# Kernel optimization log

Hardware: AMD Instinct MI355X
Metric: run time of the kernel (lower is better)

Reference implementation:

```python
import jax, jax.numpy as jnp
import numpy as np

ROWS, COLS, BATCH, NC, DEG = 256, 512, 512, 5, 16
N = (ROWS + COLS) * BATCH            # total nodes
E = ROWS * DEG * BATCH               # total edges
EPS = 1e-07

def _idx_sets():
    blk = np.arange(BATCH)[:, None] * (ROWS + COLS)
    idx_check = (blk + np.arange(ROWS)[None, :]).ravel()          # index_one
    idx_var = (blk + ROWS + np.arange(COLS)[None, :]).ravel()      # index_two
    return jnp.asarray(idx_check, jnp.int32), jnp.asarray(idx_var, jnp.int32)

IDX_CHECK, IDX_VAR = _idx_sets()

def setup_inputs() -> dict:
    key = jax.random.key(0)
    ks = jax.random.split(key, 18)
    rng = np.random.default_rng(0)
    # per-graph block offsets; row0 = check node ids, row1 = variable ids BEFORE the +ROWS shift
    offs = np.repeat(np.arange(BATCH) * (ROWS + COLS), ROWS * DEG)
    src = offs + rng.integers(0, ROWS, size=E)
    dst = offs + rng.integers(0, COLS, size=E)
    edge_index = jnp.asarray(np.stack([src, dst]), jnp.int32)
    x = jax.random.normal(ks[0], (N, 1), jnp.float32)

    def p(k, shape, fan):
        return (jax.random.uniform(k, shape, jnp.float32) * 2.0 - 1.0) / np.sqrt(fan)

    inp = {"x": x, "edge_index": edge_index}
    for li, base in ((1, 1), (2, 9)):
        inp[f"w1_{li}"] = p(ks[base + 0], (10, 2), 2)
        inp[f"b1_{li}"] = p(ks[base + 1], (10,), 2)
        inp[f"w2_{li}"] = p(ks[base + 2], (1, 10), 10)
        inp[f"b2_{li}"] = p(ks[base + 3], (1,), 10)
        inp[f"wih_{li}"] = p(ks[base + 4], (3, 1), 1)
        inp[f"whh_{li}"] = p(ks[base + 5], (3, 1), 1)
        inp[f"bih_{li}"] = p(ks[base + 6], (3,), 1)
        inp[f"bhh_{li}"] = p(ks[base + 7], (3,), 1)
    return inp

def _ggc(h, j_idx, i_idx, agg_idx, upd_idx, w1, b1, w2, b2, wih, whh, bih, bhh):
    # message: mlp(cat[x_j, x_i])
    feat = jnp.concatenate([h[j_idx], h[i_idx]], axis=1)          # [E,2]
    hid = jax.nn.relu(feat @ w1.T + b1)                            # [E,10]
    msg = hid @ w2.T + b2                                          # [E,1]
    m = jax.ops.segment_sum(msg, agg_idx, num_segments=N)          # scatter-add -> [N,1]
    # GRUCell(input=h[idx], hx=m[idx])   (note: original passes old state as INPUT, message as HIDDEN)
    xg = h[upd_idx]
    hx = m[upd_idx]
    gi = xg @ wih.T + bih                                          # [K,3]
    gh = hx @ whh.T + bhh                                          # [K,3]
    r = jax.nn.sigmoid(gi[:, 0:1] + gh[:, 0:1])
    z = jax.nn.sigmoid(gi[:, 1:2] + gh[:, 1:2])
    n = jnp.tanh(gi[:, 2:3] + r * gh[:, 2:3])
    hnew = (1.0 - z) * n + z * hx
    return h.at[upd_idx].set(hnew)

def reference(x, edge_index, w1_1, b1_1, w2_1, b2_1, wih_1, whh_1, bih_1, bhh_1,
              w1_2, b1_2, w2_2, b2_2, wih_2, whh_2, bih_2, bhh_2):
    src = edge_index[0]
    dst = edge_index[1] + ROWS          # shift variable ids into node index space
    h = x
    for _ in range(NC):
        # ggc1: source_to_target -> x_j=h[src], x_i=h[dst], aggregate at dst, update variable nodes
        h = _ggc(h, src, dst, dst, IDX_VAR, w1_1, b1_1, w2_1, b2_1, wih_1, whh_1, bih_1, bhh_1)
        # ggc2: target_to_source -> x_j=h[dst], x_i=h[src], aggregate at src, update check nodes
        h = _ggc(h, dst, src, src, IDX_CHECK, w1_2, b1_2, w2_2, b2_2, wih_2, whh_2, bih_2, bhh_2)
    return jnp.clip(jax.nn.sigmoid(-h), EPS, 1.0 - EPS)
```

## Files before the change

kernel.cpp:

```cpp
#include <hip/hip_runtime.h>

#define ROWS 256
#define COLS 512
#define BATCH 512
#define NC 5
#define DEG 16
#define EPG (ROWS * DEG)
#define NPG (ROWS + COLS)
#define NT 512
#define EPT (EPG / NT)
#define EPSF 1e-7f

typedef unsigned short u16;
typedef unsigned int   u32;
typedef float v2f __attribute__((ext_vector_type(2)));

__device__ __forceinline__ float sigmoid_f(float a) {
    return 1.0f / (1.0f + __expf(-a));
}
__device__ __forceinline__ float tanh_f(float a) {
    return fmaf(2.0f, 1.0f / (1.0f + __expf(-2.0f * a)), -1.0f);
}

__global__ __launch_bounds__(NT, 4) void gnni_kernel(
    const float* __restrict__ x,
    const int*   __restrict__ eidx,
    const float* __restrict__ w1_1, const float* __restrict__ b1_1,
    const float* __restrict__ w2_1, const float* __restrict__ b2_1,
    const float* __restrict__ wih_1, const float* __restrict__ whh_1,
    const float* __restrict__ bih_1, const float* __restrict__ bhh_1,
    const float* __restrict__ w1_2, const float* __restrict__ b1_2,
    const float* __restrict__ w2_2, const float* __restrict__ b2_2,
    const float* __restrict__ wih_2, const float* __restrict__ whh_2,
    const float* __restrict__ bih_2, const float* __restrict__ bhh_2,
    float* __restrict__ out)
{
    __shared__ float msg[EPG];
    __shared__ u32  cntd[COLS];
    __shared__ u32  cnts[ROWS];
    __shared__ u16  ofs_v[COLS + 1];
    __shared__ u16  ofs_c[ROWS + 1];
    __shared__ float hc[ROWS];
    __shared__ float hv[COLS];
    __shared__ u32  wsum[8];
    __shared__ u32  wsum2[4];

    const int tid  = threadIdx.x;
    const int lane = tid & 63;
    const int wid  = tid >> 6;
    const int b    = blockIdx.x;
    const int base = b * NPG;
    const long ebase = (long)b * EPG;

    const int4 sa = *(const int4*)(eidx + ebase + tid * 8);
    const int4 sb = *(const int4*)(eidx + ebase + tid * 8 + 4);
    const int4 da = *(const int4*)(eidx + (long)BATCH * EPG + ebase + tid * 8);
    const int4 db = *(const int4*)(eidx + (long)BATCH * EPG + ebase + tid * 8 + 4);
    const int sarr[EPT] = {sa.x, sa.y, sa.z, sa.w, sb.x, sb.y, sb.z, sb.w};
    const int darr[EPT] = {da.x, da.y, da.z, da.w, db.x, db.y, db.z, db.w};
    u32 ep[EPT];
    #pragma unroll
    for (int i = 0; i < EPT; ++i)
        ep[i] = (u32)(sarr[i] - base) | ((u32)(darr[i] - base) << 16);

    cntd[tid] = 0;
    if (tid < ROWS) cnts[tid] = 0;
    __syncthreads();
    #pragma unroll
    for (int i = 0; i < EPT; ++i) {
        atomicAdd(&cntd[ep[i] >> 16], 1u);
        atomicAdd(&cnts[ep[i] & 0xffffu], 1u);
    }
    __syncthreads();

    u32 myd = cntd[tid];
    u32 scv = myd;
    #pragma unroll
    for (int st = 1; st < 64; st <<= 1) {
        u32 t = __shfl_up(scv, st);
        if (lane >= st) scv += t;
    }
    if (lane == 63) wsum[wid] = scv;
    u32 mys = 0, scc = 0;
    if (tid < ROWS) {
        mys = cnts[tid];
        scc = mys;
        #pragma unroll
        for (int st = 1; st < 64; st <<= 1) {
            u32 t = __shfl_up(scc, st);
            if (lane >= st) scc += t;
        }
        if (lane == 63) wsum2[wid] = scc;
    }
    __syncthreads();
    if (tid < 8) {
        u32 v = wsum[tid];
        #pragma unroll
        for (int st = 1; st < 8; st <<= 1) {
            u32 t = __shfl_up(v, st);
            if (tid >= st) v += t;
        }
        wsum[tid] = v;
    } else if (tid < 12) {
        u32 v = wsum2[tid - 8];
        #pragma unroll
        for (int st = 1; st < 4; st <<= 1) {
            u32 t = __shfl_up(v, st);
            if (tid - 8 >= st) v += t;
        }
        wsum2[tid - 8] = v;
    }
    __syncthreads();
    {
        u32 inc = scv + (wid ? wsum[wid - 1] : 0u);
        ofs_v[tid + 1] = (u16)inc;
        if (tid == 0) ofs_v[0] = 0;
        cntd[tid] = inc - myd;
    }
    if (tid < ROWS) {
        u32 inc = scc + (wid ? wsum2[wid - 1] : 0u);
        ofs_c[tid + 1] = (u16)inc;
        if (tid == 0) ofs_c[0] = 0;
        cnts[tid] = inc - mys;
        hc[tid] = x[base + tid];
    }
    float hvreg = x[base + ROWS + tid];
    hv[tid] = hvreg;
    __syncthreads();

    u32 aS[EPT], aD[EPT], p1B[EPT], p2B[EPT];
    #pragma unroll
    for (int i = 0; i < EPT; ++i) {
        const u32 p = ep[i];
        const u32 s = p & 0xffffu;
        const u32 d = p >> 16;
        aS[i]  = s << 2;
        aD[i]  = d << 2;
        p1B[i] = atomicAdd(&cntd[d], 1u) << 2;
        p2B[i] = atomicAdd(&cnts[s], 1u) << 2;
    }

    v2f A1[5], C1[5], B1[5], W1[5], A2[5], C2[5], B2[5], W2[5];
    #pragma unroll
    for (int j = 0; j < 5; ++j) {
        A1[j] = (v2f){w1_1[4*j],     w1_1[4*j + 2]};
        C1[j] = (v2f){w1_1[4*j + 1], w1_1[4*j + 3]};
        B1[j] = (v2f){b1_1[2*j],     b1_1[2*j + 1]};
        W1[j] = (v2f){w2_1[2*j],     w2_1[2*j + 1]};
        A2[j] = (v2f){w1_2[4*j],     w1_2[4*j + 2]};
        C2[j] = (v2f){w1_2[4*j + 1], w1_2[4*j + 3]};
        B2[j] = (v2f){b1_2[2*j],     b1_2[2*j + 1]};
        W2[j] = (v2f){w2_2[2*j],     w2_2[2*j + 1]};
    }
    const float b2_1s = b2_1[0], b2_2s = b2_2[0];
    const v2f zero2 = (v2f){0.0f, 0.0f};
    const char* const hcB  = (const char*)hc;
    const char* const hvB  = (const char*)hv;
    char*       const msgB = (char*)msg;

    for (int it = 0; it < NC; ++it) {
        #pragma unroll
        for (int i = 0; i < EPT; ++i) {
            const float xj = *(const float*)(hcB + aS[i]);
            const float xi = *(const float*)(hvB + aD[i]);
            const v2f xj2 = (v2f){xj, xj}, xi2 = (v2f){xi, xi};
            v2f acc = (v2f){b2_1s, 0.0f};
            #pragma unroll
            for (int j = 0; j < 5; ++j) {
                v2f t = __builtin_elementwise_fma(C1[j], xi2, B1[j]);
                t = __builtin_elementwise_fma(A1[j], xj2, t);
                t = __builtin_elementwise_max(t, zero2);
                acc = __builtin_elementwise_fma(W1[j], t, acc);
            }
            *(float*)(msgB + p1B[i]) = acc.x + acc.y;
        }
        __syncthreads();

        {
            const int beg = ofs_v[tid], end = ofs_v[tid + 1];
            float hx = 0.0f;
            for (int e = beg; e < end; ++e) hx += msg[e];
            const float xg = hvreg;
            float gi0 = fmaf(wih_1[0], xg, bih_1[0]);
            float gi1 = fmaf(wih_1[1], xg, bih_1[1]);
            float gi2 = fmaf(wih_1[2], xg, bih_1[2]);
            float gh0 = fmaf(whh_1[0], hx, bhh_1[0]);
            float gh1 = fmaf(whh_1[1], hx, bhh_1[1]);
            float gh2 = fmaf(whh_1[2], hx, bhh_1[2]);
            float r = sigmoid_f(gi0 + gh0);
            float z = sigmoid_f(gi1 + gh1);
            float n = tanh_f(fmaf(r, gh2, gi2));
            hvreg = fmaf(1.0f - z, n, z * hx);
            hv[tid] = hvreg;
        }
        __syncthreads();

        #pragma unroll
        for (int i = 0; i < EPT; ++i) {
            const float xi = *(const float*)(hcB + aS[i]);
            const float xj = *(const float*)(hvB + aD[i]);
            const v2f xj2 = (v2f){xj, xj}, xi2 = (v2f){xi, xi};
            v2f acc = (v2f){b2_2s, 0.0f};
            #pragma unroll
            for (int j = 0; j < 5; ++j) {
                v2f t = __builtin_elementwise_fma(C2[j], xi2, B2[j]);
                t = __builtin_elementwise_fma(A2[j], xj2, t);
                t = __builtin_elementwise_max(t, zero2);
                acc = __builtin_elementwise_fma(W2[j], t, acc);
            }
            *(float*)(msgB + p2B[i]) = acc.x + acc.y;
        }
        __syncthreads();

        {
            const int c    = tid >> 1;
            const int half = tid & 1;
            const int beg = ofs_c[c], end = ofs_c[c + 1];
            const int h0  = (end - beg + 1) >> 1;
            const int lo  = half ? (beg + h0) : beg;
            const int hi  = half ? end : (beg + h0);
            float part = 0.0f;
            for (int e = lo; e < hi; ++e) part += msg[e];
            part += __shfl_xor(part, 1);
            if (half == 0) {
                const float hx = part;
                const float xg = hc[c];
                float gi0 = fmaf(wih_2[0], xg, bih_2[0]);
                float gi1 = fmaf(wih_2[1], xg, bih_2[1]);
                float gi2 = fmaf(wih_2[2], xg, bih_2[2]);
                float gh0 = fmaf(whh_2[0], hx, bhh_2[0]);
                float gh1 = fmaf(whh_2[1], hx, bhh_2[1]);
                float gh2 = fmaf(whh_2[2], hx, bhh_2[2]);
                float r = sigmoid_f(gi0 + gh0);
                float z = sigmoid_f(gi1 + gh1);
                float n = tanh_f(fmaf(r, gh2, gi2));
                hc[c] = fmaf(1.0f - z, n, z * hx);
            }
        }
        __syncthreads();
    }

    {
        float sgm = 1.0f / (1.0f + __expf(hvreg));
        out[base + ROWS + tid] = fminf(fmaxf(sgm, EPSF), 1.0f - EPSF);
    }
    if (tid < ROWS) {
        float sgm = 1.0f / (1.0f + __expf(hc[tid]));
        out[base + tid] = fminf(fmaxf(sgm, EPSF), 1.0f - EPSF);
    }
}

extern "C" void kernel_launch(void* const* d_in, const int* in_sizes, int n_in,
                              void* d_out, int out_size, void* d_ws, size_t ws_size,
                              hipStream_t stream) {
    const float* x    = (const float*)d_in[0];
    const int*   eidx = (const int*)d_in[1];
    gnni_kernel<<<BATCH, NT, 0, stream>>>(
        x, eidx,
        (const float*)d_in[2],  (const float*)d_in[3],
        (const float*)d_in[4],  (const float*)d_in[5],
        (const float*)d_in[6],  (const float*)d_in[7],
        (const float*)d_in[8],  (const float*)d_in[9],
        (const float*)d_in[10], (const float*)d_in[11],
        (const float*)d_in[12], (const float*)d_in[13],
        (const float*)d_in[14], (const float*)d_in[15],
        (const float*)d_in[16], (const float*)d_in[17],
        (float*)d_out);
}
```

Measured before the change: 40.58 us.

## Pad CSR segments to 4-aligned and reduce messages with float4 LDS loads

Separate message buffers are used for the variable and check aggregations. Each node's CSR segment is padded to a multiple of four and zero-filled, so the gather reductions can use unrolled float4 LDS reads with a scalar tail loop instead of per-element serial loops. The check-node h values for each edge are loaded once per iteration and reused by both message phases. This increases LDS footprint and adds zero-initialization, which could reduce occupancy.

```diff
diff --git a/kernel.cpp b/kernel.cpp
--- a/kernel.cpp
+++ b/kernel.cpp
@@ -10,6 +10,8 @@
 #define NT 512
 #define EPT (EPG / NT)
 #define EPSF 1e-7f
+#define MV_W (EPG + 3 * COLS)
+#define MC_W (EPG + 3 * ROWS)
 
 typedef unsigned short u16;
 typedef unsigned int   u32;
@@ -35,11 +37,14 @@
     const float* __restrict__ bih_2, const float* __restrict__ bhh_2,
     float* __restrict__ out)
 {
-    __shared__ float msg[EPG];
+    __shared__ float msgV[MV_W];
+    __shared__ float msgC[MC_W];
     __shared__ u32  cntd[COLS];
     __shared__ u32  cnts[ROWS];
-    __shared__ u16  ofs_v[COLS + 1];
-    __shared__ u16  ofs_c[ROWS + 1];
+    __shared__ u16  beg_v[COLS];
+    __shared__ u16  deg_v[COLS];
+    __shared__ u16  beg_c[ROWS];
+    __shared__ u16  deg_c[ROWS];
     __shared__ float hc[ROWS];
     __shared__ float hv[COLS];
     __shared__ u32  wsum[8];
@@ -63,9 +68,12 @@
     for (int i = 0; i < EPT; ++i)
         ep[i] = (u32)(sarr[i] - base) | ((u32)(darr[i] - base) << 16);
 
+    for (int i = tid; i < MV_W; i += NT) msgV[i] = 0.0f;
+    for (int i = tid; i < MC_W; i += NT) msgC[i] = 0.0f;
     cntd[tid] = 0;
     if (tid < ROWS) cnts[tid] = 0;
     __syncthreads();
+
     #pragma unroll
     for (int i = 0; i < EPT; ++i) {
         atomicAdd(&cntd[ep[i] >> 16], 1u);
@@ -74,17 +82,19 @@
     __syncthreads();
 
     u32 myd = cntd[tid];
-    u32 scv = myd;
+    u32 acd = (myd + 3u) & ~3u;
+    u32 scv = acd;
     #pragma unroll
     for (int st = 1; st < 64; st <<= 1) {
         u32 t = __shfl_up(scv, st);
         if (lane >= st) scv += t;
     }
     if (lane == 63) wsum[wid] = scv;
-    u32 mys = 0, scc = 0;
+    u32 mys = 0, acs = 0, scc = 0;
     if (tid < ROWS) {
         mys = cnts[tid];
-        scc = mys;
+        acs = (mys + 3u) & ~3u;
+        scc = acs;
         #pragma unroll
         for (int st = 1; st < 64; st <<= 1) {
             u32 t = __shfl_up(scc, st);
@@ -112,16 +122,18 @@
     }
     __syncthreads();
     {
-        u32 inc = scv + (wid ? wsum[wid - 1] : 0u);
-        ofs_v[tid + 1] = (u16)inc;
-        if (tid == 0) ofs_v[0] = 0;
-        cntd[tid] = inc - myd;
+        u32 inc  = scv + (wid ? wsum[wid - 1] : 0u);
+        u32 begv = inc - acd;
+        beg_v[tid] = (u16)begv;
+        deg_v[tid] = (u16)myd;
+        cntd[tid]  = begv;
     }
     if (tid < ROWS) {
-        u32 inc = scc + (wid ? wsum2[wid - 1] : 0u);
-        ofs_c[tid + 1] = (u16)inc;
-        if (tid == 0) ofs_c[0] = 0;
-        cnts[tid] = inc - mys;
+        u32 inc  = scc + (wid ? wsum2[wid - 1] : 0u);
+        u32 begc = inc - acs;
+        beg_c[tid] = (u16)begc;
+        deg_c[tid] = (u16)mys;
+        cnts[tid]  = begc;
         hc[tid] = x[base + tid];
     }
     float hvreg = x[base + ROWS + tid];
@@ -154,14 +166,19 @@
     }
     const float b2_1s = b2_1[0], b2_2s = b2_2[0];
     const v2f zero2 = (v2f){0.0f, 0.0f};
-    const char* const hcB  = (const char*)hc;
-    const char* const hvB  = (const char*)hv;
-    char*       const msgB = (char*)msg;
+    const char* const hcB   = (const char*)hc;
+    const char* const hvB   = (const char*)hv;
+    char*       const msgVB = (char*)msgV;
+    char*       const msgCB = (char*)msgC;
 
     for (int it = 0; it < NC; ++it) {
+        float hcs[EPT];
+        #pragma unroll
+        for (int i = 0; i < EPT; ++i) hcs[i] = *(const float*)(hcB + aS[i]);
+
         #pragma unroll
         for (int i = 0; i < EPT; ++i) {
-            const float xj = *(const float*)(hcB + aS[i]);
+            const float xj = hcs[i];
             const float xi = *(const float*)(hvB + aD[i]);
             const v2f xj2 = (v2f){xj, xj}, xi2 = (v2f){xi, xi};
             v2f acc = (v2f){b2_1s, 0.0f};
@@ -172,14 +189,24 @@
                 t = __builtin_elementwise_max(t, zero2);
                 acc = __builtin_elementwise_fma(W1[j], t, acc);
             }
-            *(float*)(msgB + p1B[i]) = acc.x + acc.y;
+            *(float*)(msgVB + p1B[i]) = acc.x + acc.y;
         }
         __syncthreads();
 
         {
-            const int beg = ofs_v[tid], end = ofs_v[tid + 1];
-            float hx = 0.0f;
-            for (int e = beg; e < end; ++e) hx += msg[e];
+            const int beg = beg_v[tid];
+            const int deg = deg_v[tid];
+            const float4* mp = (const float4*)&msgV[beg];
+            float4 a4 = {0.0f, 0.0f, 0.0f, 0.0f};
+            #pragma unroll
+            for (int k = 0; k < 5; ++k) {
+                if (4 * k < deg) {
+                    const float4 q = mp[k];
+                    a4.x += q.x; a4.y += q.y; a4.z += q.z; a4.w += q.w;
+                }
+            }
+            float hx = (a4.x + a4.y) + (a4.z + a4.w);
+            for (int e = beg + 20; e < beg + deg; ++e) hx += msgV[e];
             const float xg = hvreg;
             float gi0 = fmaf(wih_1[0], xg, bih_1[0]);
             float gi1 = fmaf(wih_1[1], xg, bih_1[1]);
@@ -197,7 +224,7 @@
 
         #pragma unroll
         for (int i = 0; i < EPT; ++i) {
-            const float xi = *(const float*)(hcB + aS[i]);
+            const float xi = hcs[i];
             const float xj = *(const float*)(hvB + aD[i]);
             const v2f xj2 = (v2f){xj, xj}, xi2 = (v2f){xi, xi};
             v2f acc = (v2f){b2_2s, 0.0f};
@@ -208,19 +235,27 @@
                 t = __builtin_elementwise_max(t, zero2);
                 acc = __builtin_elementwise_fma(W2[j], t, acc);
             }
-            *(float*)(msgB + p2B[i]) = acc.x + acc.y;
+            *(float*)(msgCB + p2B[i]) = acc.x + acc.y;
         }
         __syncthreads();
 
         {
             const int c    = tid >> 1;
             const int half = tid & 1;
-            const int beg = ofs_c[c], end = ofs_c[c + 1];
-            const int h0  = (end - beg + 1) >> 1;
-            const int lo  = half ? (beg + h0) : beg;
-            const int hi  = half ? end : (beg + h0);
-            float part = 0.0f;
-            for (int e = lo; e < hi; ++e) part += msg[e];
+            const int beg = beg_c[c];
+            const int deg = deg_c[c];
+            const float4* mp = (const float4*)&msgC[beg];
+            float4 a4 = {0.0f, 0.0f, 0.0f, 0.0f};
+            #pragma unroll
+            for (int k = 0; k < 4; ++k) {
+                const int ch = half + 2 * k;
+                if (4 * ch < deg) {
+                    const float4 q = mp[ch];
+                    a4.x += q.x; a4.y += q.y; a4.z += q.z; a4.w += q.w;
+                }
+            }
+            float part = (a4.x + a4.y) + (a4.z + a4.w);
+            for (int e = beg + 32 + half; e < beg + deg; e += 2) part += msgC[e];
             part += __shfl_xor(part, 1);
             if (half == 0) {
                 const float hx = part;
```

Result: faster. 38.44 us (-5.3%).
